# Optimization experiments

Measured on AMD Instinct MI355X. Metric: run time of the kernel, lower is better.

Reference implementation:

```python
import jax, jax.numpy as jnp
import numpy as np

N = 50000
E = 800000
HID = 128
EIN = 2 * HID + 1  # h[row] ++ h[col] ++ edge_attr
NC = 3             # n_coords
DIM = 3            # spatial dim
NORM_FACTOR = 100.0
LN_EPS = 1e-5


def layernorm(x, g, b):
    m = jnp.mean(x, axis=-1, keepdims=True)
    v = jnp.mean(jnp.square(x - m), axis=-1, keepdims=True)
    return (x - m) * jax.lax.rsqrt(v + LN_EPS) * g + b


def setup_inputs() -> dict:
    key = jax.random.key(0)
    ks = jax.random.split(key, 12)
    h = jax.random.normal(ks[0], (N, HID), dtype=jnp.float32)
    coord = jax.random.normal(ks[1], (N, NC, DIM), dtype=jnp.float32)
    coord_diff = jax.random.normal(ks[2], (E, NC, DIM), dtype=jnp.float32)
    edge_attr = jax.random.normal(ks[3], (E, 1), dtype=jnp.float32)
    edge_mask = jnp.ones((E, 1), dtype=jnp.float32)
    node_mask = jnp.ones((N, 1, 1), dtype=jnp.float32)
    row = jax.random.randint(ks[4], (E,), 0, N, dtype=jnp.int32)
    col = jax.random.randint(ks[5], (E,), 0, N, dtype=jnp.int32)
    # MLP params (stored [in, out])
    def xavier(k, fi, fo, gain=1.0):
        lim = gain * np.sqrt(6.0 / (fi + fo))
        return jax.random.uniform(k, (fi, fo), dtype=jnp.float32, minval=-lim, maxval=lim)
    W1 = xavier(ks[6], EIN, HID)
    b1 = jnp.zeros((HID,), jnp.float32)
    g1 = jnp.ones((HID,), jnp.float32)
    be1 = jnp.zeros((HID,), jnp.float32)
    W2 = xavier(ks[7], HID, HID)
    b2 = jnp.zeros((HID,), jnp.float32)
    g2 = jnp.ones((HID,), jnp.float32)
    be2 = jnp.zeros((HID,), jnp.float32)
    W3 = xavier(ks[8], HID, NC * NC, gain=0.01)  # final layer, no bias
    return dict(h=h, coord=coord, coord_diff=coord_diff, edge_attr=edge_attr,
                edge_mask=edge_mask, node_mask=node_mask, row=row, col=col,
                W1=W1, b1=b1, g1=g1, be1=be1, W2=W2, b2=b2, g2=g2, be2=be2, W3=W3)


def reference(h, coord, coord_diff, edge_attr, edge_mask, node_mask, row, col,
              W1, b1, g1, be1, W2, b2, g2, be2, W3):
    # gather node feats into edge features: [E, 2*HID + 1]
    x = jnp.concatenate([h[row], h[col], edge_attr], axis=1)
    x = jax.nn.silu(layernorm(x @ W1 + b1, g1, be1))
    x = jax.nn.silu(layernorm(x @ W2 + b2, g2, be2))
    phi = (x @ W3).reshape(-1, NC, NC)               # [E, NC, NC]
    trans = jnp.einsum('ejk,ejl->elk', coord_diff, phi)  # [E, NC, DIM]
    trans = trans * edge_mask[:, None]               # [E,1,1] broadcast
    agg = jax.ops.segment_sum(trans, row, num_segments=coord.shape[0]) / NORM_FACTOR
    return (coord + agg) * node_mask
```

## Files before the change

### kernel.cpp

```cpp
#include <hip/hip_runtime.h>
#include <hip/hip_bf16.h>

#define NN 50000
#define EE 800000

typedef __attribute__((ext_vector_type(8))) short short8;
typedef __attribute__((ext_vector_type(4))) short short4v;
typedef __attribute__((ext_vector_type(4))) float f32x4;

__device__ __forceinline__ float bf2f(ushort u) {
  union { unsigned u; float f; } v; v.u = ((unsigned)u) << 16; return v.f;
}
__device__ __forceinline__ ushort f2bf(float f) {
  union { float f; unsigned u; } v; v.f = f;
  unsigned r = v.u + 0x7FFFu + ((v.u >> 16) & 1u);
  return (ushort)(r >> 16);
}
__device__ __forceinline__ float silu(float v) {
  return v * __builtin_amdgcn_rcpf(1.f + __expf(-v));
}

__global__ void prep_kernel(const float* __restrict__ h, ushort* __restrict__ hb,
                            const float* __restrict__ W1, const float* __restrict__ W2,
                            const float* __restrict__ W3,
                            ushort* __restrict__ W1t, ushort* __restrict__ W2t,
                            ushort* __restrict__ W3t, float* __restrict__ agg) {
  int b = blockIdx.x, tid = threadIdx.x;
  if (b < 3125) {
    int i = b * 256 + tid;
    const float4* p = (const float4*)h;
    float4 a = p[2*i], c = p[2*i+1];
    short8 o;
    o[0]=f2bf(a.x); o[1]=f2bf(a.y); o[2]=f2bf(a.z); o[3]=f2bf(a.w);
    o[4]=f2bf(c.x); o[5]=f2bf(c.y); o[6]=f2bf(c.z); o[7]=f2bf(c.w);
    *(short8*)(hb + 8*i) = o;
  } else if (b < 3325) {
    int i = (b - 3125) * 256 + tid;
    if (i < 32768) {
      int n = i >> 8, k = i & 255;
      W1t[i] = f2bf(W1[k*128 + n]);
    } else if (i < 49152) {
      int j = i - 32768, n = j >> 7, k = j & 127;
      W2t[j] = f2bf(W2[k*128 + n]);
    } else if (i < 51200) {
      int j = i - 49152, n = j >> 7, k = j & 127;
      W3t[j] = (n < 9) ? f2bf(W3[k*9 + n]) : (ushort)0;
    }
  } else {
    int i = (b - 3325) * 256 + tid;
    if (i < NN*9) agg[i] = 0.f;
  }
}

template<bool USE_HB>
__global__ __launch_bounds__(256, 4)
void edge_kernel(const float* __restrict__ h, const ushort* __restrict__ hb,
                 const ushort* __restrict__ W1t, const ushort* __restrict__ W2t,
                 const ushort* __restrict__ W3t,
                 const float* __restrict__ W1,
                 const float* __restrict__ b1, const float* __restrict__ g1, const float* __restrict__ be1,
                 const float* __restrict__ b2, const float* __restrict__ g2, const float* __restrict__ be2,
                 const float* __restrict__ edge_attr, const float* __restrict__ edge_mask,
                 const float* __restrict__ coord_diff,
                 const int* __restrict__ row, const int* __restrict__ col,
                 float* __restrict__ agg) {
  __shared__ __align__(16) char smem[36864];
  ushort* smA   = (ushort*)smem;
  ushort* smX   = (ushort*)smem;
  float*  smPhi = (float*)(smem + 16384);
  float*  smCd  = (float*)(smem + 32768);
  float*  smEA  = (float*)(smem + 35072);
  float*  smEM  = (float*)(smem + 35328);
  int*    smRow = (int*)  (smem + 35584);
  float2* smRed = (float2*)(smem + 35840);

  const int tid  = threadIdx.x;
  const int lane = tid & 63;
  const int w    = tid >> 6;
  const int l15  = lane & 15;
  const int lh   = lane >> 4;
  const int wm   = w >> 1;
  const int wn   = w & 1;
  const int e0   = blockIdx.x * 64;

  const int nb = wm*64 + lh*4;

  {
    int e = tid >> 2, p = tid & 3;
    int re = row[e0 + e], ce = col[e0 + e];
    if (p == 0) { smEA[e] = edge_attr[e0+e]; smEM[e] = edge_mask[e0+e]; smRow[e] = re; }
    if (USE_HB) {
      const ushort* s = hb + (size_t)((p & 2) ? ce : re) * 128 + (p & 1) * 64;
      #pragma unroll
      for (int c = 0; c < 8; ++c) {
        short8 v = *(const short8*)(s + c*8);
        int bo = (e*512 + (p*8 + c)*16) ^ ((e & 7) << 4);
        *(short8*)((char*)smA + bo) = v;
      }
    } else {
      const float* s = h + (size_t)((p & 2) ? ce : re) * 128 + (p & 1) * 64;
      #pragma unroll
      for (int c = 0; c < 8; ++c) {
        float4 a = *(const float4*)(s + c*8);
        float4 bq = *(const float4*)(s + c*8 + 4);
        short8 v;
        v[0]=f2bf(a.x); v[1]=f2bf(a.y); v[2]=f2bf(a.z); v[3]=f2bf(a.w);
        v[4]=f2bf(bq.x); v[5]=f2bf(bq.y); v[6]=f2bf(bq.z); v[7]=f2bf(bq.w);
        int bo = (e*512 + (p*8 + c)*16) ^ ((e & 7) << 4);
        *(short8*)((char*)smA + bo) = v;
      }
    }
  }
  if (tid < 144)
    *(float4*)(smCd + tid*4) = *(const float4*)(coord_diff + (size_t)e0*9 + tid*4);
  __syncthreads();

  f32x4 acc[4][2] = {};
  {
    const ushort* A0 = W1t + (size_t)(wm*64 + l15) * 256 + lh*8;
    #pragma unroll
    for (int k0 = 0; k0 < 8; ++k0) {
      short8 a[4], b[2];
      #pragma unroll
      for (int mf = 0; mf < 4; ++mf) a[mf] = *(const short8*)(A0 + mf*4096 + k0*32);
      #pragma unroll
      for (int nf = 0; nf < 2; ++nf) {
        int e = wn*32 + nf*16 + l15;
        int bo = (e*512 + k0*64 + lh*16) ^ ((e & 7) << 4);
        b[nf] = *(const short8*)((char*)smA + bo);
      }
      #pragma unroll
      for (int mf = 0; mf < 4; ++mf)
        #pragma unroll
        for (int nf = 0; nf < 2; ++nf)
          acc[mf][nf] = __builtin_amdgcn_mfma_f32_16x16x32_bf16(a[mf], b[nf], acc[mf][nf], 0, 0, 0);
    }
  }

  float s[2] = {0.f, 0.f}, q[2] = {0.f, 0.f};
  {
    const float* wl = W1 + 256*128;
    float ea[2];
    #pragma unroll
    for (int nf = 0; nf < 2; ++nf) ea[nf] = smEA[wn*32 + nf*16 + l15];
    #pragma unroll
    for (int mf = 0; mf < 4; ++mf) {
      float4 b1q = *(const float4*)(b1 + nb + mf*16);
      float4 wlq = *(const float4*)(wl + nb + mf*16);
      #pragma unroll
      for (int nf = 0; nf < 2; ++nf)
        #pragma unroll
        for (int j = 0; j < 4; ++j) {
          float t = acc[mf][nf][j] + ((const float*)&b1q)[j] + ea[nf] * ((const float*)&wlq)[j];
          acc[mf][nf][j] = t; s[nf] += t; q[nf] += t*t;
        }
    }
  }
  #pragma unroll
  for (int nf = 0; nf < 2; ++nf) {
    s[nf] += __shfl_xor(s[nf], 16, 64); s[nf] += __shfl_xor(s[nf], 32, 64);
    q[nf] += __shfl_xor(q[nf], 16, 64); q[nf] += __shfl_xor(q[nf], 32, 64);
  }
  if (lh == 0) {
    #pragma unroll
    for (int nf = 0; nf < 2; ++nf)
      smRed[((wm*2 + wn)*2 + nf)*16 + l15] = make_float2(s[nf], q[nf]);
  }
  __syncthreads();

  {
    float m[2], rs[2];
    #pragma unroll
    for (int nf = 0; nf < 2; ++nf) {
      float2 po = smRed[(((wm^1)*2 + wn)*2 + nf)*16 + l15];
      float S = s[nf] + po.x, Q = q[nf] + po.y;
      m[nf] = S * (1.f/128.f);
      rs[nf] = rsqrtf(Q * (1.f/128.f) - m[nf]*m[nf] + 1e-5f);
    }
    #pragma unroll
    for (int mf = 0; mf < 4; ++mf) {
      float4 gq  = *(const float4*)(g1 + nb + mf*16);
      float4 beq = *(const float4*)(be1 + nb + mf*16);
      #pragma unroll
      for (int nf = 0; nf < 2; ++nf) {
        int e = wn*32 + nf*16 + l15;
        short4v o;
        #pragma unroll
        for (int j = 0; j < 4; ++j) {
          float val = (acc[mf][nf][j] - m[nf]) * rs[nf] * ((const float*)&gq)[j] + ((const float*)&beq)[j];
          o[j] = f2bf(silu(val));
        }
        int bo = (e*256 + (nb + mf*16)*2) ^ ((e & 7) << 4);
        *(short4v*)((char*)smX + bo) = o;
      }
    }
  }
  __syncthreads();

  f32x4 acc2[4][2] = {};
  {
    const ushort* A2 = W2t + (size_t)(wm*64 + l15) * 128 + lh*8;
    #pragma unroll
    for (int k0 = 0; k0 < 4; ++k0) {
      short8 a[4], b[2];
      #pragma unroll
      for (int mf = 0; mf < 4; ++mf) a[mf] = *(const short8*)(A2 + mf*2048 + k0*32);
      #pragma unroll
      for (int nf = 0; nf < 2; ++nf) {
        int e = wn*32 + nf*16 + l15;
        int bo = (e*256 + k0*64 + lh*16) ^ ((e & 7) << 4);
        b[nf] = *(const short8*)((char*)smX + bo);
      }
      #pragma unroll
      for (int mf = 0; mf < 4; ++mf)
        #pragma unroll
        for (int nf = 0; nf < 2; ++nf)
          acc2[mf][nf] = __builtin_amdgcn_mfma_f32_16x16x32_bf16(a[mf], b[nf], acc2[mf][nf], 0, 0, 0);
    }
  }

  float s2[2] = {0.f, 0.f}, q2[2] = {0.f, 0.f};
  #pragma unroll
  for (int mf = 0; mf < 4; ++mf) {
    float4 b2q = *(const float4*)(b2 + nb + mf*16);
    #pragma unroll
    for (int nf = 0; nf < 2; ++nf)
      #pragma unroll
      for (int j = 0; j < 4; ++j) {
        float t = acc2[mf][nf][j] + ((const float*)&b2q)[j];
        acc2[mf][nf][j] = t; s2[nf] += t; q2[nf] += t*t;
      }
  }
  #pragma unroll
  for (int nf = 0; nf < 2; ++nf) {
    s2[nf] += __shfl_xor(s2[nf], 16, 64); s2[nf] += __shfl_xor(s2[nf], 32, 64);
    q2[nf] += __shfl_xor(q2[nf], 16, 64); q2[nf] += __shfl_xor(q2[nf], 32, 64);
  }
  if (lh == 0) {
    #pragma unroll
    for (int nf = 0; nf < 2; ++nf)
      smRed[((wm*2 + wn)*2 + nf)*16 + l15] = make_float2(s2[nf], q2[nf]);
  }
  __syncthreads();

  {
    float m[2], rs[2];
    #pragma unroll
    for (int nf = 0; nf < 2; ++nf) {
      float2 po = smRed[(((wm^1)*2 + wn)*2 + nf)*16 + l15];
      float S = s2[nf] + po.x, Q = q2[nf] + po.y;
      m[nf] = S * (1.f/128.f);
      rs[nf] = rsqrtf(Q * (1.f/128.f) - m[nf]*m[nf] + 1e-5f);
    }
    #pragma unroll
    for (int mf = 0; mf < 4; ++mf) {
      float4 gq  = *(const float4*)(g2 + nb + mf*16);
      float4 beq = *(const float4*)(be2 + nb + mf*16);
      #pragma unroll
      for (int nf = 0; nf < 2; ++nf) {
        int e = wn*32 + nf*16 + l15;
        short4v o;
        #pragma unroll
        for (int j = 0; j < 4; ++j) {
          float val = (acc2[mf][nf][j] - m[nf]) * rs[nf] * ((const float*)&gq)[j] + ((const float*)&beq)[j];
          o[j] = f2bf(silu(val));
        }
        int bo = (e*256 + (nb + mf*16)*2) ^ ((e & 7) << 4);
        *(short4v*)((char*)smX + bo) = o;
      }
    }
  }
  __syncthreads();

  {
    f32x4 acc3 = {};
    const ushort* A3 = W3t + (size_t)l15 * 128 + lh*8;
    int e = w*16 + l15;
    #pragma unroll
    for (int k0 = 0; k0 < 4; ++k0) {
      short8 a = *(const short8*)(A3 + k0*32);
      int bo = (e*256 + k0*64 + lh*16) ^ ((e & 7) << 4);
      short8 b = *(const short8*)((char*)smX + bo);
      acc3 = __builtin_amdgcn_mfma_f32_16x16x32_bf16(a, b, acc3, 0, 0, 0);
    }
    *(float4*)(smPhi + e*20 + lh*4) = *(float4*)&acc3;
  }
  __syncthreads();

  {
    int e = tid >> 2, qd = tid & 3;
    int re = smRow[e];
    float em = smEM[e];
    const float* cd = smCd + e*9;
    const float* ph = smPhi + e*20;
    for (int idx = qd; idx < 9; idx += 4) {
      int l2 = idx / 3, k = idx - l2*3;
      float t = cd[k]*ph[l2] + cd[3+k]*ph[3+l2] + cd[6+k]*ph[6+l2];
      unsafeAtomicAdd(&agg[(size_t)re*9 + idx], t * em);
    }
  }
}

__global__ void finalize_kernel(const float* __restrict__ coord, const float* __restrict__ node_mask,
                                const float* __restrict__ agg, float* __restrict__ out) {
  int i = blockIdx.x * 256 + threadIdx.x;
  if (i < NN*9) {
    int n = i / 9;
    out[i] = (coord[i] + agg[i] * 0.01f) * node_mask[n];
  }
}

extern "C" void kernel_launch(void* const* d_in, const int* in_sizes, int n_in,
                              void* d_out, int out_size, void* d_ws, size_t ws_size,
                              hipStream_t stream) {
  const float* h          = (const float*)d_in[0];
  const float* coord      = (const float*)d_in[1];
  const float* coord_diff = (const float*)d_in[2];
  const float* edge_attr  = (const float*)d_in[3];
  const float* edge_mask  = (const float*)d_in[4];
  const float* node_mask  = (const float*)d_in[5];
  const int*   rowi       = (const int*)d_in[6];
  const int*   coli       = (const int*)d_in[7];
  const float* W1  = (const float*)d_in[8];
  const float* b1  = (const float*)d_in[9];
  const float* g1  = (const float*)d_in[10];
  const float* be1 = (const float*)d_in[11];
  const float* W2  = (const float*)d_in[12];
  const float* b2  = (const float*)d_in[13];
  const float* g2  = (const float*)d_in[14];
  const float* be2 = (const float*)d_in[15];
  const float* W3  = (const float*)d_in[16];

  char* ws = (char*)d_ws;
  float*  agg = (float*)ws;
  ushort* W1t = (ushort*)(ws + 1800064);
  ushort* W2t = (ushort*)(ws + 1865600);
  ushort* W3t = (ushort*)(ws + 1898368);
  ushort* hb  = (ushort*)(ws + 1902464);
  bool use_hb = ws_size >= (size_t)1902464 + 12800000;

  prep_kernel<<<3325 + (NN*9 + 255)/256, 256, 0, stream>>>(h, hb, W1, W2, W3, W1t, W2t, W3t, agg);
  if (use_hb) {
    edge_kernel<true><<<EE/64, 256, 0, stream>>>(h, hb, W1t, W2t, W3t, W1,
        b1, g1, be1, b2, g2, be2, edge_attr, edge_mask, coord_diff, rowi, coli, agg);
  } else {
    edge_kernel<false><<<EE/64, 256, 0, stream>>>(h, hb, W1t, W2t, W3t, W1,
        b1, g1, be1, b2, g2, be2, edge_attr, edge_mask, coord_diff, rowi, coli, agg);
  }
  finalize_kernel<<<(NN*9 + 255)/256, 256, 0, stream>>>(coord, node_mask, agg, (float*)d_out);
}
```

Measured before the change: 508.8 us.

## Make each wave own 32 edges end-to-end and drop block barriers

The edge MLP is restructured so each wave processes its own 32 edges across all 128 output features. Gathered node features now load straight from global memory into MFMA operand registers, with no shared-memory staging. Because a wave holds whole rows, LayerNorm statistics reduce within the wave, so all __syncthreads and cross-wave reductions are removed. Each block now handles 128 edges, and launch bounds drop to 3 waves per SIMD to make room for the doubled accumulator register footprint. The risks are lower occupancy, and every wave reloading the full W1/W2 fragments from global or L2 instead of splitting them across waves.

After: 548.1 us. 7.7% more time.

```diff
diff --git a/kernel.cpp b/kernel.cpp
--- a/kernel.cpp
+++ b/kernel.cpp
@@ -53,7 +53,7 @@
 }
 
 template<bool USE_HB>
-__global__ __launch_bounds__(256, 4)
+__global__ __launch_bounds__(256, 3)
 void edge_kernel(const float* __restrict__ h, const ushort* __restrict__ hb,
                  const ushort* __restrict__ W1t, const ushort* __restrict__ W2t,
                  const ushort* __restrict__ W3t,
@@ -64,94 +64,73 @@
                  const float* __restrict__ coord_diff,
                  const int* __restrict__ row, const int* __restrict__ col,
                  float* __restrict__ agg) {
-  __shared__ __align__(16) char smem[36864];
-  ushort* smA   = (ushort*)smem;
-  ushort* smX   = (ushort*)smem;
-  float*  smPhi = (float*)(smem + 16384);
-  float*  smCd  = (float*)(smem + 32768);
-  float*  smEA  = (float*)(smem + 35072);
-  float*  smEM  = (float*)(smem + 35328);
-  int*    smRow = (int*)  (smem + 35584);
-  float2* smRed = (float2*)(smem + 35840);
-
+  __shared__ __align__(16) char smem[4 * 12032];
   const int tid  = threadIdx.x;
   const int lane = tid & 63;
   const int w    = tid >> 6;
   const int l15  = lane & 15;
   const int lh   = lane >> 4;
-  const int wm   = w >> 1;
-  const int wn   = w & 1;
-  const int e0   = blockIdx.x * 64;
-
-  const int nb = wm*64 + lh*4;
-
-  {
-    int e = tid >> 2, p = tid & 3;
-    int re = row[e0 + e], ce = col[e0 + e];
-    if (p == 0) { smEA[e] = edge_attr[e0+e]; smEM[e] = edge_mask[e0+e]; smRow[e] = re; }
-    if (USE_HB) {
-      const ushort* s = hb + (size_t)((p & 2) ? ce : re) * 128 + (p & 1) * 64;
-      #pragma unroll
-      for (int c = 0; c < 8; ++c) {
-        short8 v = *(const short8*)(s + c*8);
-        int bo = (e*512 + (p*8 + c)*16) ^ ((e & 7) << 4);
-        *(short8*)((char*)smA + bo) = v;
-      }
-    } else {
-      const float* s = h + (size_t)((p & 2) ? ce : re) * 128 + (p & 1) * 64;
-      #pragma unroll
-      for (int c = 0; c < 8; ++c) {
-        float4 a = *(const float4*)(s + c*8);
-        float4 bq = *(const float4*)(s + c*8 + 4);
-        short8 v;
-        v[0]=f2bf(a.x); v[1]=f2bf(a.y); v[2]=f2bf(a.z); v[3]=f2bf(a.w);
-        v[4]=f2bf(bq.x); v[5]=f2bf(bq.y); v[6]=f2bf(bq.z); v[7]=f2bf(bq.w);
-        int bo = (e*512 + (p*8 + c)*16) ^ ((e & 7) << 4);
-        *(short8*)((char*)smA + bo) = v;
-      }
-    }
-  }
-  if (tid < 144)
-    *(float4*)(smCd + tid*4) = *(const float4*)(coord_diff + (size_t)e0*9 + tid*4);
-  __syncthreads();
-
-  f32x4 acc[4][2] = {};
-  {
-    const ushort* A0 = W1t + (size_t)(wm*64 + l15) * 256 + lh*8;
-    #pragma unroll
-    for (int k0 = 0; k0 < 8; ++k0) {
-      short8 a[4], b[2];
-      #pragma unroll
-      for (int mf = 0; mf < 4; ++mf) a[mf] = *(const short8*)(A0 + mf*4096 + k0*32);
-      #pragma unroll
-      for (int nf = 0; nf < 2; ++nf) {
-        int e = wn*32 + nf*16 + l15;
-        int bo = (e*512 + k0*64 + lh*16) ^ ((e & 7) << 4);
-        b[nf] = *(const short8*)((char*)smA + bo);
-      }
-      #pragma unroll
-      for (int mf = 0; mf < 4; ++mf)
-        #pragma unroll
-        for (int nf = 0; nf < 2; ++nf)
-          acc[mf][nf] = __builtin_amdgcn_mfma_f32_16x16x32_bf16(a[mf], b[nf], acc[mf][nf], 0, 0, 0);
-    }
-  }
-
-  float s[2] = {0.f, 0.f}, q[2] = {0.f, 0.f};
+
+  char*  wb     = smem + w * 12032;
+  ushort* xbuf  = (ushort*)wb;
+  float*  cdbuf = (float*)(wb + 8192);
+  float*  phibuf= (float*)(wb + 9472);
+
+  const int we0 = (blockIdx.x * 4 + w) * 32;
+
+  int rn[2], cn[2]; float ea[2], em[2];
+  #pragma unroll
+  for (int nf = 0; nf < 2; ++nf) {
+    int e = we0 + nf*16 + l15;
+    rn[nf] = row[e]; cn[nf] = col[e];
+    ea[nf] = edge_attr[e]; em[nf] = edge_mask[e];
+  }
+  {
+    const float* cdsrc = coord_diff + (size_t)we0 * 9;
+    *(float4*)(cdbuf + lane*4) = *(const float4*)(cdsrc + lane*4);
+    if (lane < 8)
+      *(float4*)(cdbuf + 256 + lane*4) = *(const float4*)(cdsrc + 256 + lane*4);
+  }
+
+  f32x4 acc[8][2] = {};
+  #pragma unroll
+  for (int k0 = 0; k0 < 8; ++k0) {
+    short8 b[2];
+    #pragma unroll
+    for (int nf = 0; nf < 2; ++nf) {
+      int node = (k0 < 4) ? rn[nf] : cn[nf];
+      int koff = (k0 & 3)*32 + lh*8;
+      if (USE_HB) {
+        b[nf] = *(const short8*)(hb + (size_t)node*128 + koff);
+      } else {
+        const float* s = h + (size_t)node*128 + koff;
+        float4 u = *(const float4*)s, vq = *(const float4*)(s + 4);
+        short8 t;
+        t[0]=f2bf(u.x); t[1]=f2bf(u.y); t[2]=f2bf(u.z); t[3]=f2bf(u.w);
+        t[4]=f2bf(vq.x); t[5]=f2bf(vq.y); t[6]=f2bf(vq.z); t[7]=f2bf(vq.w);
+        b[nf] = t;
+      }
+    }
+    #pragma unroll
+    for (int mf = 0; mf < 8; ++mf) {
+      short8 a = *(const short8*)(W1t + (size_t)(mf*16 + l15)*256 + k0*32 + lh*8);
+      acc[mf][0] = __builtin_amdgcn_mfma_f32_16x16x32_bf16(a, b[0], acc[mf][0], 0, 0, 0);
+      acc[mf][1] = __builtin_amdgcn_mfma_f32_16x16x32_bf16(a, b[1], acc[mf][1], 0, 0, 0);
+    }
+  }
+
+  float s[2] = {0.f,0.f}, q[2] = {0.f,0.f};
   {
     const float* wl = W1 + 256*128;
-    float ea[2];
-    #pragma unroll
-    for (int nf = 0; nf < 2; ++nf) ea[nf] = smEA[wn*32 + nf*16 + l15];
-    #pragma unroll
-    for (int mf = 0; mf < 4; ++mf) {
-      float4 b1q = *(const float4*)(b1 + nb + mf*16);
-      float4 wlq = *(const float4*)(wl + nb + mf*16);
+    #pragma unroll
+    for (int mf = 0; mf < 8; ++mf) {
+      float4 bq = *(const float4*)(b1 + mf*16 + lh*4);
+      float4 wq = *(const float4*)(wl + mf*16 + lh*4);
       #pragma unroll
       for (int nf = 0; nf < 2; ++nf)
         #pragma unroll
         for (int j = 0; j < 4; ++j) {
-          float t = acc[mf][nf][j] + ((const float*)&b1q)[j] + ea[nf] * ((const float*)&wlq)[j];
+          float t = acc[mf][nf][j] + ((const float*)&bq)[j] + ea[nf] * ((const float*)&wq)[j];
           acc[mf][nf][j] = t; s[nf] += t; q[nf] += t*t;
         }
     }
@@ -161,73 +140,57 @@
     s[nf] += __shfl_xor(s[nf], 16, 64); s[nf] += __shfl_xor(s[nf], 32, 64);
     q[nf] += __shfl_xor(q[nf], 16, 64); q[nf] += __shfl_xor(q[nf], 32, 64);
   }
-  if (lh == 0) {
-    #pragma unroll
-    for (int nf = 0; nf < 2; ++nf)
-      smRed[((wm*2 + wn)*2 + nf)*16 + l15] = make_float2(s[nf], q[nf]);
-  }
-  __syncthreads();
-
   {
     float m[2], rs[2];
     #pragma unroll
     for (int nf = 0; nf < 2; ++nf) {
-      float2 po = smRed[(((wm^1)*2 + wn)*2 + nf)*16 + l15];
-      float S = s[nf] + po.x, Q = q[nf] + po.y;
-      m[nf] = S * (1.f/128.f);
-      rs[nf] = rsqrtf(Q * (1.f/128.f) - m[nf]*m[nf] + 1e-5f);
-    }
-    #pragma unroll
-    for (int mf = 0; mf < 4; ++mf) {
-      float4 gq  = *(const float4*)(g1 + nb + mf*16);
-      float4 beq = *(const float4*)(be1 + nb + mf*16);
+      m[nf]  = s[nf] * (1.f/128.f);
+      rs[nf] = rsqrtf(q[nf] * (1.f/128.f) - m[nf]*m[nf] + 1e-5f);
+    }
+    #pragma unroll
+    for (int mf = 0; mf < 8; ++mf) {
+      float4 gq  = *(const float4*)(g1 + mf*16 + lh*4);
+      float4 beq = *(const float4*)(be1 + mf*16 + lh*4);
       #pragma unroll
       for (int nf = 0; nf < 2; ++nf) {
-        int e = wn*32 + nf*16 + l15;
+        int e32 = nf*16 + l15;
         short4v o;
         #pragma unroll
         for (int j = 0; j < 4; ++j) {
           float val = (acc[mf][nf][j] - m[nf]) * rs[nf] * ((const float*)&gq)[j] + ((const float*)&beq)[j];
           o[j] = f2bf(silu(val));
         }
-        int bo = (e*256 + (nb + mf*16)*2) ^ ((e & 7) << 4);
-        *(short4v*)((char*)smX + bo) = o;
-      }
-    }
-  }
-  __syncthreads();
-
-  f32x4 acc2[4][2] = {};
-  {
-    const ushort* A2 = W2t + (size_t)(wm*64 + l15) * 128 + lh*8;
-    #pragma unroll
-    for (int k0 = 0; k0 < 4; ++k0) {
-      short8 a[4], b[2];
-      #pragma unroll
-      for (int mf = 0; mf < 4; ++mf) a[mf] = *(const short8*)(A2 + mf*2048 + k0*32);
-      #pragma unroll
-      for (int nf = 0; nf < 2; ++nf) {
-        int e = wn*32 + nf*16 + l15;
-        int bo = (e*256 + k0*64 + lh*16) ^ ((e & 7) << 4);
-        b[nf] = *(const short8*)((char*)smX + bo);
-      }
-      #pragma unroll
-      for (int mf = 0; mf < 4; ++mf)
-        #pragma unroll
-        for (int nf = 0; nf < 2; ++nf)
-          acc2[mf][nf] = __builtin_amdgcn_mfma_f32_16x16x32_bf16(a[mf], b[nf], acc2[mf][nf], 0, 0, 0);
-    }
-  }
-
-  float s2[2] = {0.f, 0.f}, q2[2] = {0.f, 0.f};
-  #pragma unroll
-  for (int mf = 0; mf < 4; ++mf) {
-    float4 b2q = *(const float4*)(b2 + nb + mf*16);
+        *(short4v*)((char*)xbuf + ((mf*2 + (lh>>1))*32 + e32)*16 + (lh&1)*8) = o;
+      }
+    }
+  }
+
+  f32x4 acc2[8][2] = {};
+  #pragma unroll
+  for (int k0 = 0; k0 < 4; ++k0) {
+    short8 b[2];
+    #pragma unroll
+    for (int nf = 0; nf < 2; ++nf) {
+      int e32 = nf*16 + l15;
+      b[nf] = *(const short8*)((char*)xbuf + ((k0*4 + lh)*32 + e32)*16);
+    }
+    #pragma unroll
+    for (int mf = 0; mf < 8; ++mf) {
+      short8 a = *(const short8*)(W2t + (size_t)(mf*16 + l15)*128 + k0*32 + lh*8);
+      acc2[mf][0] = __builtin_amdgcn_mfma_f32_16x16x32_bf16(a, b[0], acc2[mf][0], 0, 0, 0);
+      acc2[mf][1] = __builtin_amdgcn_mfma_f32_16x16x32_bf16(a, b[1], acc2[mf][1], 0, 0, 0);
+    }
+  }
+
+  float s2[2] = {0.f,0.f}, q2[2] = {0.f,0.f};
+  #pragma unroll
+  for (int mf = 0; mf < 8; ++mf) {
+    float4 bq = *(const float4*)(b2 + mf*16 + lh*4);
     #pragma unroll
     for (int nf = 0; nf < 2; ++nf)
       #pragma unroll
       for (int j = 0; j < 4; ++j) {
-        float t = acc2[mf][nf][j] + ((const float*)&b2q)[j];
+        float t = acc2[mf][nf][j] + ((const float*)&bq)[j];
         acc2[mf][nf][j] = t; s2[nf] += t; q2[nf] += t*t;
       }
   }
@@ -236,67 +199,63 @@
     s2[nf] += __shfl_xor(s2[nf], 16, 64); s2[nf] += __shfl_xor(s2[nf], 32, 64);
     q2[nf] += __shfl_xor(q2[nf], 16, 64); q2[nf] += __shfl_xor(q2[nf], 32, 64);
   }
-  if (lh == 0) {
-    #pragma unroll
-    for (int nf = 0; nf < 2; ++nf)
-      smRed[((wm*2 + wn)*2 + nf)*16 + l15] = make_float2(s2[nf], q2[nf]);
-  }
-  __syncthreads();
-
   {
     float m[2], rs[2];
     #pragma unroll
     for (int nf = 0; nf < 2; ++nf) {
-      float2 po = smRed[(((wm^1)*2 + wn)*2 + nf)*16 + l15];
-      float S = s2[nf] + po.x, Q = q2[nf] + po.y;
-      m[nf] = S * (1.f/128.f);
-      rs[nf] = rsqrtf(Q * (1.f/128.f) - m[nf]*m[nf] + 1e-5f);
-    }
-    #pragma unroll
-    for (int mf = 0; mf < 4; ++mf) {
-      float4 gq  = *(const float4*)(g2 + nb + mf*16);
-      float4 beq = *(const float4*)(be2 + nb + mf*16);
+      m[nf]  = s2[nf] * (1.f/128.f);
+      rs[nf] = rsqrtf(q2[nf] * (1.f/128.f) - m[nf]*m[nf] + 1e-5f);
+    }
+    #pragma unroll
+    for (int mf = 0; mf < 8; ++mf) {
+      float4 gq  = *(const float4*)(g2 + mf*16 + lh*4);
+      float4 beq = *(const float4*)(be2 + mf*16 + lh*4);
       #pragma unroll
       for (int nf = 0; nf < 2; ++nf) {
-        int e = wn*32 + nf*16 + l15;
+        int e32 = nf*16 + l15;
         short4v o;
         #pragma unroll
         for (int j = 0; j < 4; ++j) {
           float val = (acc2[mf][nf][j] - m[nf]) * rs[nf] * ((const float*)&gq)[j] + ((const float*)&beq)[j];
           o[j] = f2bf(silu(val));
         }
-        int bo = (e*256 + (nb + mf*16)*2) ^ ((e & 7) << 4);
-        *(short4v*)((char*)smX + bo) = o;
-      }
-    }
-  }
-  __syncthreads();
-
-  {
-    f32x4 acc3 = {};
-    const ushort* A3 = W3t + (size_t)l15 * 128 + lh*8;
-    int e = w*16 + l15;
+        *(short4v*)((char*)xbuf + ((mf*2 + (lh>>1))*32 + e32)*16 + (lh&1)*8) = o;
+      }
+    }
+  }
+
+  {
+    f32x4 acc3[2] = {};
     #pragma unroll
     for (int k0 = 0; k0 < 4; ++k0) {
-      short8 a = *(const short8*)(A3 + k0*32);
-      int bo = (e*256 + k0*64 + lh*16) ^ ((e & 7) << 4);
-      short8 b = *(const short8*)((char*)smX + bo);
-      acc3 = __builtin_amdgcn_mfma_f32_16x16x32_bf16(a, b, acc3, 0, 0, 0);
-    }
-    *(float4*)(smPhi + e*20 + lh*4) = *(float4*)&acc3;
-  }
-  __syncthreads();
-
-  {
-    int e = tid >> 2, qd = tid & 3;
-    int re = smRow[e];
-    float em = smEM[e];
-    const float* cd = smCd + e*9;
-    const float* ph = smPhi + e*20;
-    for (int idx = qd; idx < 9; idx += 4) {
-      int l2 = idx / 3, k = idx - l2*3;
-      float t = cd[k]*ph[l2] + cd[3+k]*ph[3+l2] + cd[6+k]*ph[6+l2];
-      unsafeAtomicAdd(&agg[(size_t)re*9 + idx], t * em);
+      short8 a = *(const short8*)(W3t + (size_t)l15*128 + k0*32 + lh*8);
+      #pragma unroll
+      for (int nf = 0; nf < 2; ++nf) {
+        int e32 = nf*16 + l15;
+        short8 b = *(const short8*)((char*)xbuf + ((k0*4 + lh)*32 + e32)*16);
+        acc3[nf] = __builtin_amdgcn_mfma_f32_16x16x32_bf16(a, b, acc3[nf], 0, 0, 0);
+      }
+    }
+    #pragma unroll
+    for (int nf = 0; nf < 2; ++nf) {
+      int e32 = nf*16 + l15;
+      *(f32x4*)(phibuf + e32*20 + lh*4) = acc3[nf];
+    }
+  }
+
+  if (lh < 3) {
+    #pragma unroll
+    for (int nf = 0; nf < 2; ++nf) {
+      int e32 = nf*16 + l15;
+      const float* cdp = cdbuf + e32*9;
+      const float* php = phibuf + e32*20;
+      int re = rn[nf]; float emv = em[nf];
+      int l = lh;
+      #pragma unroll
+      for (int k = 0; k < 3; ++k) {
+        float t = cdp[k]*php[l] + cdp[3+k]*php[3+l] + cdp[6+k]*php[6+l];
+        unsafeAtomicAdd(&agg[(size_t)re*9 + l*3 + k], t * emv);
+      }
     }
   }
 }
@@ -341,10 +300,10 @@
 
   prep_kernel<<<3325 + (NN*9 + 255)/256, 256, 0, stream>>>(h, hb, W1, W2, W3, W1t, W2t, W3t, agg);
   if (use_hb) {
-    edge_kernel<true><<<EE/64, 256, 0, stream>>>(h, hb, W1t, W2t, W3t, W1,
+    edge_kernel<true><<<EE/128, 256, 0, stream>>>(h, hb, W1t, W2t, W3t, W1,
         b1, g1, be1, b2, g2, be2, edge_attr, edge_mask, coord_diff, rowi, coli, agg);
   } else {
-    edge_kernel<false><<<EE/64, 256, 0, stream>>>(h, hb, W1t, W2t, W3t, W1,
+    edge_kernel<false><<<EE/128, 256, 0, stream>>>(h, hb, W1t, W2t, W3t, W1,
         b1, g1, be1, b2, g2, be2, edge_attr, edge_mask, coord_diff, rowi, coli, agg);
   }
   finalize_kernel<<<(NN*9 + 255)/256, 256, 0, stream>>>(coord, node_mask, agg, (float*)d_out);
```

## Replace atomic scatter with linked-list per-node gather of edge contributions

Applied to the files above, without the earlier changes.

When the workspace is large enough, edges are linked per destination node through an atomicExch-built linked list. The edge kernel writes per-edge translation components to a channel-major buffer instead of doing float atomics into agg. A gather kernel then walks each node's list to sum contributions and writes the final output directly. This removes 7.2M float atomics and the separate finalize pass. In exchange it adds a list-build kernel, 28.8MB of extra stores, and pointer-chasing reads with random access into the transc buffer.

After: 666.1 us. 1.31x slower.

```diff
diff --git a/kernel.cpp b/kernel.cpp
--- a/kernel.cpp
+++ b/kernel.cpp
@@ -24,9 +24,10 @@
                             const float* __restrict__ W1, const float* __restrict__ W2,
                             const float* __restrict__ W3,
                             ushort* __restrict__ W1t, ushort* __restrict__ W2t,
-                            ushort* __restrict__ W3t, float* __restrict__ agg) {
+                            ushort* __restrict__ W3t,
+                            int* __restrict__ zmem, int zval, int zcount, int hb_blocks) {
   int b = blockIdx.x, tid = threadIdx.x;
-  if (b < 3125) {
+  if (b < hb_blocks) {
     int i = b * 256 + tid;
     const float4* p = (const float4*)h;
     float4 a = p[2*i], c = p[2*i+1];
@@ -34,8 +35,8 @@
     o[0]=f2bf(a.x); o[1]=f2bf(a.y); o[2]=f2bf(a.z); o[3]=f2bf(a.w);
     o[4]=f2bf(c.x); o[5]=f2bf(c.y); o[6]=f2bf(c.z); o[7]=f2bf(c.w);
     *(short8*)(hb + 8*i) = o;
-  } else if (b < 3325) {
-    int i = (b - 3125) * 256 + tid;
+  } else if (b < hb_blocks + 200) {
+    int i = (b - hb_blocks) * 256 + tid;
     if (i < 32768) {
       int n = i >> 8, k = i & 255;
       W1t[i] = f2bf(W1[k*128 + n]);
@@ -47,12 +48,18 @@
       W3t[j] = (n < 9) ? f2bf(W3[k*9 + n]) : (ushort)0;
     }
   } else {
-    int i = (b - 3325) * 256 + tid;
-    if (i < NN*9) agg[i] = 0.f;
-  }
-}
-
-template<bool USE_HB>
+    int i = (b - hb_blocks - 200) * 256 + tid;
+    if (i < zcount) zmem[i] = zval;
+  }
+}
+
+__global__ void build_kernel(const int* __restrict__ row, int* __restrict__ head,
+                             int* __restrict__ nxt) {
+  int i = blockIdx.x * 256 + threadIdx.x;
+  if (i < EE) nxt[i] = atomicExch(&head[row[i]], i);
+}
+
+template<int MODE>
 __global__ __launch_bounds__(256, 4)
 void edge_kernel(const float* __restrict__ h, const ushort* __restrict__ hb,
                  const ushort* __restrict__ W1t, const ushort* __restrict__ W2t,
@@ -63,7 +70,7 @@
                  const float* __restrict__ edge_attr, const float* __restrict__ edge_mask,
                  const float* __restrict__ coord_diff,
                  const int* __restrict__ row, const int* __restrict__ col,
-                 float* __restrict__ agg) {
+                 float* __restrict__ agg, float* __restrict__ transc) {
   __shared__ __align__(16) char smem[36864];
   ushort* smA   = (ushort*)smem;
   ushort* smX   = (ushort*)smem;
@@ -82,14 +89,13 @@
   const int wm   = w >> 1;
   const int wn   = w & 1;
   const int e0   = blockIdx.x * 64;
-
-  const int nb = wm*64 + lh*4;
+  const int nb   = wm*64 + lh*4;
 
   {
     int e = tid >> 2, p = tid & 3;
     int re = row[e0 + e], ce = col[e0 + e];
     if (p == 0) { smEA[e] = edge_attr[e0+e]; smEM[e] = edge_mask[e0+e]; smRow[e] = re; }
-    if (USE_HB) {
+    if (MODE < 2) {
       const ushort* s = hb + (size_t)((p & 2) ? ce : re) * 128 + (p & 1) * 64;
       #pragma unroll
       for (int c = 0; c < 8; ++c) {
@@ -287,7 +293,20 @@
   }
   __syncthreads();
 
-  {
+  if (MODE == 0) {
+    #pragma unroll
+    for (int it = 0; it < 3; ++it) {
+      int idx = it*256 + tid;
+      if (idx < 576) {
+        int c = idx >> 6, e = idx & 63;
+        int l2 = c / 3, k = c - l2*3;
+        const float* cd = smCd + e*9;
+        const float* ph = smPhi + e*20;
+        float t = cd[k]*ph[l2] + cd[3+k]*ph[3+l2] + cd[6+k]*ph[6+l2];
+        transc[(size_t)c*EE + e0 + e] = t * smEM[e];
+      }
+    }
+  } else {
     int e = tid >> 2, qd = tid & 3;
     int re = smRow[e];
     float em = smEM[e];
@@ -299,6 +318,19 @@
       unsafeAtomicAdd(&agg[(size_t)re*9 + idx], t * em);
     }
   }
+}
+
+__global__ void gather_kernel(const float* __restrict__ coord, const float* __restrict__ node_mask,
+                              const float* __restrict__ transc, const int* __restrict__ head,
+                              const int* __restrict__ nxt, float* __restrict__ out) {
+  int i = blockIdx.x * 256 + threadIdx.x;
+  if (i >= 9*NN) return;
+  int c = i / NN;
+  int n = i - c*NN;
+  const float* slice = transc + (size_t)c*EE;
+  float sum = 0.f;
+  for (int e = head[n]; e >= 0; e = nxt[e]) sum += slice[e];
+  out[n*9 + c] = (coord[n*9 + c] + sum * 0.01f) * node_mask[n];
 }
 
 __global__ void finalize_kernel(const float* __restrict__ coord, const float* __restrict__ node_mask,
@@ -332,20 +364,46 @@
   const float* W3  = (const float*)d_in[16];
 
   char* ws = (char*)d_ws;
-  float*  agg = (float*)ws;
-  ushort* W1t = (ushort*)(ws + 1800064);
-  ushort* W2t = (ushort*)(ws + 1865600);
-  ushort* W3t = (ushort*)(ws + 1898368);
-  ushort* hb  = (ushort*)(ws + 1902464);
-  bool use_hb = ws_size >= (size_t)1902464 + 12800000;
-
-  prep_kernel<<<3325 + (NN*9 + 255)/256, 256, 0, stream>>>(h, hb, W1, W2, W3, W1t, W2t, W3t, agg);
-  if (use_hb) {
-    edge_kernel<true><<<EE/64, 256, 0, stream>>>(h, hb, W1t, W2t, W3t, W1,
-        b1, g1, be1, b2, g2, be2, edge_attr, edge_mask, coord_diff, rowi, coli, agg);
+  const size_t needA = 45102400;
+  const size_t needB = (size_t)1902464 + 12800000;
+  if (ws_size >= needA) {
+    float* transc = (float*)ws;
+    int*   head   = (int*)(ws + 28800000);
+    int*   nxt    = (int*)(ws + 29000000);
+    ushort* W1t   = (ushort*)(ws + 32200000);
+    ushort* W2t   = (ushort*)(ws + 32265536);
+    ushort* W3t   = (ushort*)(ws + 32298304);
+    ushort* hb    = (ushort*)(ws + 32302400);
+    prep_kernel<<<3125 + 200 + 196, 256, 0, stream>>>(h, hb, W1, W2, W3, W1t, W2t, W3t,
+                                                      head, -1, NN, 3125);
+    build_kernel<<<EE/256, 256, 0, stream>>>(rowi, head, nxt);
+    edge_kernel<0><<<EE/64, 256, 0, stream>>>(h, hb, W1t, W2t, W3t, W1,
+        b1, g1, be1, b2, g2, be2, edge_attr, edge_mask, coord_diff, rowi, coli,
+        nullptr, transc);
+    gather_kernel<<<(9*NN + 255)/256, 256, 0, stream>>>(coord, node_mask, transc, head, nxt,
+                                                        (float*)d_out);
+  } else if (ws_size >= needB) {
+    float*  agg = (float*)ws;
+    ushort* W1t = (ushort*)(ws + 1800064);
+    ushort* W2t = (ushort*)(ws + 1865600);
+    ushort* W3t = (ushort*)(ws + 1898368);
+    ushort* hb  = (ushort*)(ws + 1902464);
+    prep_kernel<<<3125 + 200 + 1758, 256, 0, stream>>>(h, hb, W1, W2, W3, W1t, W2t, W3t,
+                                                       (int*)agg, 0, NN*9, 3125);
+    edge_kernel<1><<<EE/64, 256, 0, stream>>>(h, hb, W1t, W2t, W3t, W1,
+        b1, g1, be1, b2, g2, be2, edge_attr, edge_mask, coord_diff, rowi, coli,
+        agg, nullptr);
+    finalize_kernel<<<(NN*9 + 255)/256, 256, 0, stream>>>(coord, node_mask, agg, (float*)d_out);
   } else {
-    edge_kernel<false><<<EE/64, 256, 0, stream>>>(h, hb, W1t, W2t, W3t, W1,
-        b1, g1, be1, b2, g2, be2, edge_attr, edge_mask, coord_diff, rowi, coli, agg);
-  }
-  finalize_kernel<<<(NN*9 + 255)/256, 256, 0, stream>>>(coord, node_mask, agg, (float*)d_out);
-}
+    float*  agg = (float*)ws;
+    ushort* W1t = (ushort*)(ws + 1800064);
+    ushort* W2t = (ushort*)(ws + 1865600);
+    ushort* W3t = (ushort*)(ws + 1898368);
+    prep_kernel<<<200 + 1758, 256, 0, stream>>>(h, nullptr, W1, W2, W3, W1t, W2t, W3t,
+                                                (int*)agg, 0, NN*9, 0);
+    edge_kernel<2><<<EE/64, 256, 0, stream>>>(h, nullptr, W1t, W2t, W3t, W1,
+        b1, g1, be1, b2, g2, be2, edge_attr, edge_mask, coord_diff, rowi, coli,
+        agg, nullptr);
+    finalize_kernel<<<(NN*9 + 255)/256, 256, 0, stream>>>(coord, node_mask, agg, (float*)d_out);
+  }
+}
```

## Precompute per-node first-layer projections and gather them per edge instead

Applied to the files above, without the earlier changes.

Splits W1 into row and col halves and computes h@W1a+b1 and h@W1b once per node in a new node kernel. The edge kernel then gathers these two projections and adds the edge_attr term directly, removing the first per-edge GEMM (16x fewer MACs for that layer). LayerNorm 1 is now done per thread in registers with a quad shuffle reduction, and shared memory drops, so occupancy is raised to 6 blocks. The cost is larger gather traffic (fp32 or bf16 projections of 128 values per endpoint) and an extra kernel launch.

After: 536.3 us. 1.05x slower.

```diff
diff --git a/kernel.cpp b/kernel.cpp
--- a/kernel.cpp
+++ b/kernel.cpp
@@ -20,25 +20,20 @@
   return v * __builtin_amdgcn_rcpf(1.f + __expf(-v));
 }
 
-__global__ void prep_kernel(const float* __restrict__ h, ushort* __restrict__ hb,
-                            const float* __restrict__ W1, const float* __restrict__ W2,
+__global__ void prep_kernel(const float* __restrict__ W1, const float* __restrict__ W2,
                             const float* __restrict__ W3,
-                            ushort* __restrict__ W1t, ushort* __restrict__ W2t,
-                            ushort* __restrict__ W3t, float* __restrict__ agg) {
+                            ushort* __restrict__ W1at, ushort* __restrict__ W1bt,
+                            ushort* __restrict__ W2t, ushort* __restrict__ W3t,
+                            float* __restrict__ agg) {
   int b = blockIdx.x, tid = threadIdx.x;
-  if (b < 3125) {
+  if (b < 200) {
     int i = b * 256 + tid;
-    const float4* p = (const float4*)h;
-    float4 a = p[2*i], c = p[2*i+1];
-    short8 o;
-    o[0]=f2bf(a.x); o[1]=f2bf(a.y); o[2]=f2bf(a.z); o[3]=f2bf(a.w);
-    o[4]=f2bf(c.x); o[5]=f2bf(c.y); o[6]=f2bf(c.z); o[7]=f2bf(c.w);
-    *(short8*)(hb + 8*i) = o;
-  } else if (b < 3325) {
-    int i = (b - 3125) * 256 + tid;
-    if (i < 32768) {
-      int n = i >> 8, k = i & 255;
-      W1t[i] = f2bf(W1[k*128 + n]);
+    if (i < 16384) {
+      int n = i >> 7, k = i & 127;
+      W1at[i] = f2bf(W1[k*128 + n]);
+    } else if (i < 32768) {
+      int j = i - 16384, n = j >> 7, k = j & 127;
+      W1bt[j] = f2bf(W1[(k + 128)*128 + n]);
     } else if (i < 49152) {
       int j = i - 32768, n = j >> 7, k = j & 127;
       W2t[j] = f2bf(W2[k*128 + n]);
@@ -47,32 +42,105 @@
       W3t[j] = (n < 9) ? f2bf(W3[k*9 + n]) : (ushort)0;
     }
   } else {
-    int i = (b - 3325) * 256 + tid;
+    int i = (b - 200) * 256 + tid;
     if (i < NN*9) agg[i] = 0.f;
   }
 }
 
-template<bool USE_HB>
+template<bool PQF32>
 __global__ __launch_bounds__(256, 4)
-void edge_kernel(const float* __restrict__ h, const ushort* __restrict__ hb,
-                 const ushort* __restrict__ W1t, const ushort* __restrict__ W2t,
-                 const ushort* __restrict__ W3t,
-                 const float* __restrict__ W1,
-                 const float* __restrict__ b1, const float* __restrict__ g1, const float* __restrict__ be1,
+void node_kernel(const float* __restrict__ h,
+                 const ushort* __restrict__ W1at, const ushort* __restrict__ W1bt,
+                 const float* __restrict__ b1,
+                 void* __restrict__ Pv, void* __restrict__ Qv) {
+  __shared__ __align__(16) ushort smH[64*128];
+  const int tid = threadIdx.x;
+  const int lane = tid & 63;
+  const int w   = tid >> 6;
+  const int l15 = lane & 15;
+  const int lh  = lane >> 4;
+  const int wm  = w >> 1;
+  const int wn  = w & 1;
+  const int n0  = blockIdx.x * 64;
+
+  {
+    int e = tid >> 2, p = tid & 3;
+    int nn = n0 + e; if (nn >= NN) nn = NN - 1;
+    const float* s = h + (size_t)nn*128 + p*32;
+    #pragma unroll
+    for (int c = 0; c < 4; ++c) {
+      float4 a = *(const float4*)(s + c*8);
+      float4 bq = *(const float4*)(s + c*8 + 4);
+      short8 v;
+      v[0]=f2bf(a.x); v[1]=f2bf(a.y); v[2]=f2bf(a.z); v[3]=f2bf(a.w);
+      v[4]=f2bf(bq.x); v[5]=f2bf(bq.y); v[6]=f2bf(bq.z); v[7]=f2bf(bq.w);
+      int bo = (e*256 + p*64 + c*16) ^ ((e & 7) << 4);
+      *(short8*)((char*)smH + bo) = v;
+    }
+  }
+  __syncthreads();
+
+  const ushort* W = wm ? W1bt : W1at;
+  f32x4 acc[4][2] = {};
+  #pragma unroll
+  for (int k0 = 0; k0 < 4; ++k0) {
+    short8 a[4], b[2];
+    #pragma unroll
+    for (int mf = 0; mf < 4; ++mf)
+      a[mf] = *(const short8*)(W + (size_t)(mf*16 + l15)*128 + k0*32 + lh*8);
+    #pragma unroll
+    for (int nf = 0; nf < 2; ++nf) {
+      int e = wn*32 + nf*16 + l15;
+      int bo = (e*256 + k0*64 + lh*16) ^ ((e & 7) << 4);
+      b[nf] = *(const short8*)((char*)smH + bo);
+    }
+    #pragma unroll
+    for (int mf = 0; mf < 4; ++mf)
+      #pragma unroll
+      for (int nf = 0; nf < 2; ++nf)
+        acc[mf][nf] = __builtin_amdgcn_mfma_f32_16x16x32_bf16(a[mf], b[nf], acc[mf][nf], 0, 0, 0);
+  }
+
+  #pragma unroll
+  for (int mf = 0; mf < 4; ++mf) {
+    float4 bq = *(const float4*)(b1 + mf*16 + lh*4);
+    #pragma unroll
+    for (int nf = 0; nf < 2; ++nf) {
+      int node = n0 + wn*32 + nf*16 + l15;
+      if (node < NN) {
+        f32x4 r = acc[mf][nf];
+        if (wm == 0) { r[0]+=bq.x; r[1]+=bq.y; r[2]+=bq.z; r[3]+=bq.w; }
+        if (PQF32) {
+          float* dst = (float*)(wm ? Qv : Pv) + (size_t)node*128 + mf*16 + lh*4;
+          *(f32x4*)dst = r;
+        } else {
+          ushort* dst = (ushort*)(wm ? Qv : Pv) + (size_t)node*128 + mf*16 + lh*4;
+          short4v o; o[0]=f2bf(r[0]); o[1]=f2bf(r[1]); o[2]=f2bf(r[2]); o[3]=f2bf(r[3]);
+          *(short4v*)dst = o;
+        }
+      }
+    }
+  }
+}
+
+template<bool PQF32>
+__global__ __launch_bounds__(256, 6)
+void edge_kernel(const void* __restrict__ Pv, const void* __restrict__ Qv,
+                 const float* __restrict__ w1last,
+                 const float* __restrict__ g1, const float* __restrict__ be1,
+                 const ushort* __restrict__ W2t, const ushort* __restrict__ W3t,
                  const float* __restrict__ b2, const float* __restrict__ g2, const float* __restrict__ be2,
                  const float* __restrict__ edge_attr, const float* __restrict__ edge_mask,
                  const float* __restrict__ coord_diff,
                  const int* __restrict__ row, const int* __restrict__ col,
                  float* __restrict__ agg) {
-  __shared__ __align__(16) char smem[36864];
-  ushort* smA   = (ushort*)smem;
+  __shared__ __align__(16) char smem[25344];
   ushort* smX   = (ushort*)smem;
   float*  smPhi = (float*)(smem + 16384);
-  float*  smCd  = (float*)(smem + 32768);
-  float*  smEA  = (float*)(smem + 35072);
-  float*  smEM  = (float*)(smem + 35328);
-  int*    smRow = (int*)  (smem + 35584);
-  float2* smRed = (float2*)(smem + 35840);
+  float*  smCd  = (float*)(smem + 21504);
+  float2* smRed = (float2*)(smem + 23808);
+  float*  smEM  = (float*)(smem + 24832);
+  int*    smRow = (int*)  (smem + 25088);
 
   const int tid  = threadIdx.x;
   const int lane = tid & 63;
@@ -82,119 +150,70 @@
   const int wm   = w >> 1;
   const int wn   = w & 1;
   const int e0   = blockIdx.x * 64;
-
-  const int nb = wm*64 + lh*4;
+  const int nb   = wm*64 + lh*4;
 
   {
     int e = tid >> 2, p = tid & 3;
     int re = row[e0 + e], ce = col[e0 + e];
-    if (p == 0) { smEA[e] = edge_attr[e0+e]; smEM[e] = edge_mask[e0+e]; smRow[e] = re; }
-    if (USE_HB) {
-      const ushort* s = hb + (size_t)((p & 2) ? ce : re) * 128 + (p & 1) * 64;
+    float ea = edge_attr[e0 + e];
+    if (p == 0) { smEM[e] = edge_mask[e0+e]; smRow[e] = re; }
+
+    float v[32]; float s = 0.f, q = 0.f;
+    if (PQF32) {
+      const float* Pp = (const float*)Pv + (size_t)re*128 + p*32;
+      const float* Qp = (const float*)Qv + (size_t)ce*128 + p*32;
       #pragma unroll
       for (int c = 0; c < 8; ++c) {
-        short8 v = *(const short8*)(s + c*8);
-        int bo = (e*512 + (p*8 + c)*16) ^ ((e & 7) << 4);
-        *(short8*)((char*)smA + bo) = v;
+        float4 a = *(const float4*)(Pp + c*4);
+        float4 bq = *(const float4*)(Qp + c*4);
+        float4 wq = *(const float4*)(w1last + p*32 + c*4);
+        #pragma unroll
+        for (int j = 0; j < 4; ++j) {
+          float t = ((const float*)&a)[j] + ((const float*)&bq)[j] + ea * ((const float*)&wq)[j];
+          v[c*4 + j] = t; s += t; q += t*t;
+        }
       }
     } else {
-      const float* s = h + (size_t)((p & 2) ? ce : re) * 128 + (p & 1) * 64;
-      #pragma unroll
-      for (int c = 0; c < 8; ++c) {
-        float4 a = *(const float4*)(s + c*8);
-        float4 bq = *(const float4*)(s + c*8 + 4);
-        short8 v;
-        v[0]=f2bf(a.x); v[1]=f2bf(a.y); v[2]=f2bf(a.z); v[3]=f2bf(a.w);
-        v[4]=f2bf(bq.x); v[5]=f2bf(bq.y); v[6]=f2bf(bq.z); v[7]=f2bf(bq.w);
-        int bo = (e*512 + (p*8 + c)*16) ^ ((e & 7) << 4);
-        *(short8*)((char*)smA + bo) = v;
-      }
+      const ushort* Pp = (const ushort*)Pv + (size_t)re*128 + p*32;
+      const ushort* Qp = (const ushort*)Qv + (size_t)ce*128 + p*32;
+      #pragma unroll
+      for (int c = 0; c < 4; ++c) {
+        short8 a = *(const short8*)(Pp + c*8);
+        short8 bq = *(const short8*)(Qp + c*8);
+        float4 wq0 = *(const float4*)(w1last + p*32 + c*8);
+        float4 wq1 = *(const float4*)(w1last + p*32 + c*8 + 4);
+        #pragma unroll
+        for (int j = 0; j < 8; ++j) {
+          float wv = (j < 4) ? ((const float*)&wq0)[j] : ((const float*)&wq1)[j-4];
+          float t = bf2f((ushort)a[j]) + bf2f((ushort)bq[j]) + ea * wv;
+          v[c*8 + j] = t; s += t; q += t*t;
+        }
+      }
+    }
+    s += __shfl_xor(s, 1, 64); s += __shfl_xor(s, 2, 64);
+    q += __shfl_xor(q, 1, 64); q += __shfl_xor(q, 2, 64);
+    float m  = s * (1.f/128.f);
+    float rs = rsqrtf(q * (1.f/128.f) - m*m + 1e-5f);
+    #pragma unroll
+    for (int c = 0; c < 4; ++c) {
+      float4 gq0 = *(const float4*)(g1 + p*32 + c*8);
+      float4 gq1 = *(const float4*)(g1 + p*32 + c*8 + 4);
+      float4 bq0 = *(const float4*)(be1 + p*32 + c*8);
+      float4 bq1 = *(const float4*)(be1 + p*32 + c*8 + 4);
+      short8 o;
+      #pragma unroll
+      for (int j = 0; j < 8; ++j) {
+        float gv = (j < 4) ? ((const float*)&gq0)[j] : ((const float*)&gq1)[j-4];
+        float bv = (j < 4) ? ((const float*)&bq0)[j] : ((const float*)&bq1)[j-4];
+        float val = (v[c*8+j] - m) * rs * gv + bv;
+        o[j] = f2bf(silu(val));
+      }
+      int bo = (e*256 + p*64 + c*16) ^ ((e & 7) << 4);
+      *(short8*)((char*)smX + bo) = o;
     }
   }
   if (tid < 144)
     *(float4*)(smCd + tid*4) = *(const float4*)(coord_diff + (size_t)e0*9 + tid*4);
-  __syncthreads();
-
-  f32x4 acc[4][2] = {};
-  {
-    const ushort* A0 = W1t + (size_t)(wm*64 + l15) * 256 + lh*8;
-    #pragma unroll
-    for (int k0 = 0; k0 < 8; ++k0) {
-      short8 a[4], b[2];
-      #pragma unroll
-      for (int mf = 0; mf < 4; ++mf) a[mf] = *(const short8*)(A0 + mf*4096 + k0*32);
-      #pragma unroll
-      for (int nf = 0; nf < 2; ++nf) {
-        int e = wn*32 + nf*16 + l15;
-        int bo = (e*512 + k0*64 + lh*16) ^ ((e & 7) << 4);
-        b[nf] = *(const short8*)((char*)smA + bo);
-      }
-      #pragma unroll
-      for (int mf = 0; mf < 4; ++mf)
-        #pragma unroll
-        for (int nf = 0; nf < 2; ++nf)
-          acc[mf][nf] = __builtin_amdgcn_mfma_f32_16x16x32_bf16(a[mf], b[nf], acc[mf][nf], 0, 0, 0);
-    }
-  }
-
-  float s[2] = {0.f, 0.f}, q[2] = {0.f, 0.f};
-  {
-    const float* wl = W1 + 256*128;
-    float ea[2];
-    #pragma unroll
-    for (int nf = 0; nf < 2; ++nf) ea[nf] = smEA[wn*32 + nf*16 + l15];
-    #pragma unroll
-    for (int mf = 0; mf < 4; ++mf) {
-      float4 b1q = *(const float4*)(b1 + nb + mf*16);
-      float4 wlq = *(const float4*)(wl + nb + mf*16);
-      #pragma unroll
-      for (int nf = 0; nf < 2; ++nf)
-        #pragma unroll
-        for (int j = 0; j < 4; ++j) {
-          float t = acc[mf][nf][j] + ((const float*)&b1q)[j] + ea[nf] * ((const float*)&wlq)[j];
-          acc[mf][nf][j] = t; s[nf] += t; q[nf] += t*t;
-        }
-    }
-  }
-  #pragma unroll
-  for (int nf = 0; nf < 2; ++nf) {
-    s[nf] += __shfl_xor(s[nf], 16, 64); s[nf] += __shfl_xor(s[nf], 32, 64);
-    q[nf] += __shfl_xor(q[nf], 16, 64); q[nf] += __shfl_xor(q[nf], 32, 64);
-  }
-  if (lh == 0) {
-    #pragma unroll
-    for (int nf = 0; nf < 2; ++nf)
-      smRed[((wm*2 + wn)*2 + nf)*16 + l15] = make_float2(s[nf], q[nf]);
-  }
-  __syncthreads();
-
-  {
-    float m[2], rs[2];
-    #pragma unroll
-    for (int nf = 0; nf < 2; ++nf) {
-      float2 po = smRed[(((wm^1)*2 + wn)*2 + nf)*16 + l15];
-      float S = s[nf] + po.x, Q = q[nf] + po.y;
-      m[nf] = S * (1.f/128.f);
-      rs[nf] = rsqrtf(Q * (1.f/128.f) - m[nf]*m[nf] + 1e-5f);
-    }
-    #pragma unroll
-    for (int mf = 0; mf < 4; ++mf) {
-      float4 gq  = *(const float4*)(g1 + nb + mf*16);
-      float4 beq = *(const float4*)(be1 + nb + mf*16);
-      #pragma unroll
-      for (int nf = 0; nf < 2; ++nf) {
-        int e = wn*32 + nf*16 + l15;
-        short4v o;
-        #pragma unroll
-        for (int j = 0; j < 4; ++j) {
-          float val = (acc[mf][nf][j] - m[nf]) * rs[nf] * ((const float*)&gq)[j] + ((const float*)&beq)[j];
-          o[j] = f2bf(silu(val));
-        }
-        int bo = (e*256 + (nb + mf*16)*2) ^ ((e & 7) << 4);
-        *(short4v*)((char*)smX + bo) = o;
-      }
-    }
-  }
   __syncthreads();
 
   f32x4 acc2[4][2] = {};
@@ -330,22 +349,38 @@
   const float* g2  = (const float*)d_in[14];
   const float* be2 = (const float*)d_in[15];
   const float* W3  = (const float*)d_in[16];
+  const float* w1last = W1 + 256*128;
 
   char* ws = (char*)d_ws;
-  float*  agg = (float*)ws;
-  ushort* W1t = (ushort*)(ws + 1800064);
-  ushort* W2t = (ushort*)(ws + 1865600);
-  ushort* W3t = (ushort*)(ws + 1898368);
-  ushort* hb  = (ushort*)(ws + 1902464);
-  bool use_hb = ws_size >= (size_t)1902464 + 12800000;
-
-  prep_kernel<<<3325 + (NN*9 + 255)/256, 256, 0, stream>>>(h, hb, W1, W2, W3, W1t, W2t, W3t, agg);
-  if (use_hb) {
-    edge_kernel<true><<<EE/64, 256, 0, stream>>>(h, hb, W1t, W2t, W3t, W1,
-        b1, g1, be1, b2, g2, be2, edge_attr, edge_mask, coord_diff, rowi, coli, agg);
+  const size_t needF32 = 53102400;
+  const int nodeBlocks = (NN + 63) / 64;
+  const int aggBlocks  = (NN*9 + 255) / 256;
+
+  if (ws_size >= needF32) {
+    float*  P    = (float*)ws;
+    float*  Q    = (float*)(ws + 25600000);
+    float*  agg  = (float*)(ws + 51200000);
+    ushort* W1at = (ushort*)(ws + 53000000);
+    ushort* W1bt = (ushort*)(ws + 53032768);
+    ushort* W2t  = (ushort*)(ws + 53065536);
+    ushort* W3t  = (ushort*)(ws + 53098304);
+    prep_kernel<<<200 + aggBlocks, 256, 0, stream>>>(W1, W2, W3, W1at, W1bt, W2t, W3t, agg);
+    node_kernel<true><<<nodeBlocks, 256, 0, stream>>>(h, W1at, W1bt, b1, P, Q);
+    edge_kernel<true><<<EE/64, 256, 0, stream>>>(P, Q, w1last, g1, be1, W2t, W3t,
+        b2, g2, be2, edge_attr, edge_mask, coord_diff, rowi, coli, agg);
+    finalize_kernel<<<aggBlocks, 256, 0, stream>>>(coord, node_mask, agg, (float*)d_out);
   } else {
-    edge_kernel<false><<<EE/64, 256, 0, stream>>>(h, hb, W1t, W2t, W3t, W1,
-        b1, g1, be1, b2, g2, be2, edge_attr, edge_mask, coord_diff, rowi, coli, agg);
-  }
-  finalize_kernel<<<(NN*9 + 255)/256, 256, 0, stream>>>(coord, node_mask, agg, (float*)d_out);
-}
+    ushort* P    = (ushort*)ws;
+    ushort* Q    = (ushort*)(ws + 12800000);
+    float*  agg  = (float*)(ws + 25600000);
+    ushort* W1at = (ushort*)(ws + 27400000);
+    ushort* W1bt = (ushort*)(ws + 27432768);
+    ushort* W2t  = (ushort*)(ws + 27465536);
+    ushort* W3t  = (ushort*)(ws + 27498304);
+    prep_kernel<<<200 + aggBlocks, 256, 0, stream>>>(W1, W2, W3, W1at, W1bt, W2t, W3t, agg);
+    node_kernel<false><<<nodeBlocks, 256, 0, stream>>>(h, W1at, W1bt, b1, P, Q);
+    edge_kernel<false><<<EE/64, 256, 0, stream>>>(P, Q, w1last, g1, be1, W2t, W3t,
+        b2, g2, be2, edge_attr, edge_mask, coord_diff, rowi, coli, agg);
+    finalize_kernel<<<aggBlocks, 256, 0, stream>>>(coord, node_mask, agg, (float*)d_out);
+  }
+}
```
